# Optimization experiments

Hardware: AMD Instinct MI355X
Metric: run time of the kernel (lower is better)

The kernel has to match this reference:

```python
import jax, jax.numpy as jnp
import numpy as np

B, N, D, H, M, O = 8, 1024, 256, 512, 256, 256


def _mlp(x, W1, b1, W2, b2):
    # two-layer MLP: Linear -> ReLU -> Linear (torch Linear: x @ W.T + b)
    return jax.nn.relu(x @ W1.T + b1) @ W2.T + b2


def _lstm(x, W_ih, W_hh, b):
    # x: [B, N, D] -> h: [B, N, H]; single-layer unidirectional LSTM, torch gate order i,f,g,o
    Bt, Nt, _ = x.shape
    x_proj = x @ W_ih.T + b  # [B, N, 4H] precompute input projection

    def step(carry, xt):
        h, c = carry
        gates = xt + h @ W_hh.T
        i, f, g, o = jnp.split(gates, 4, axis=-1)
        i, f, o = jax.nn.sigmoid(i), jax.nn.sigmoid(f), jax.nn.sigmoid(o)
        c = f * c + i * jnp.tanh(g)
        h = o * jnp.tanh(c)
        return (h, c), h

    h0 = jnp.zeros((Bt, W_hh.shape[1]), x.dtype)
    (_, _), hs = jax.lax.scan(step, (h0, h0), jnp.swapaxes(x_proj, 0, 1))
    return jnp.swapaxes(hs, 0, 1)


def setup_inputs() -> dict:
    key = jax.random.key(0)
    ks = jax.random.split(key, 32)
    p = lambda k, s: jax.random.normal(k, s, jnp.float32) * 0.02
    inp = {
        "feats": jax.random.normal(ks[0], (B, N, D), jnp.float32),
        "adj": jax.random.randint(ks[1], (B, N, N), 0, 2, jnp.int32),
        "W_ih": p(ks[2], (4 * H, D)),
        "W_hh": p(ks[3], (4 * H, H)),
        "b_ih": jnp.zeros((4 * H,), jnp.float32),
        "b_hh": jnp.zeros((4 * H,), jnp.float32),
        "gx_W1": p(ks[4], (M, H)), "gx_b1": jnp.zeros((M,), jnp.float32),
        "gx_W2": p(ks[5], (M, M)), "gx_b2": jnp.zeros((M,), jnp.float32),
        "gz_W1": p(ks[6], (M, H)), "gz_b1": jnp.zeros((M,), jnp.float32),
        "gz_W2": p(ks[7], (M, M)), "gz_b2": jnp.zeros((M,), jnp.float32),
        "gv_W1": p(ks[8], (M, H)), "gv_b1": jnp.zeros((M,), jnp.float32),
        "gv_W2": p(ks[9], (M, M)), "gv_b2": jnp.zeros((M,), jnp.float32),
        "gn_W1": p(ks[10], (M, M)), "gn_b1": jnp.zeros((M,), jnp.float32),
        "gn_W2": p(ks[11], (O, M)), "gn_b2": jnp.zeros((O,), jnp.float32),
        "out_W": p(ks[12], (O, H + O)), "out_b": jnp.zeros((O,), jnp.float32),
    }
    return inp


def reference(feats, adj, W_ih, W_hh, b_ih, b_hh,
              gx_W1, gx_b1, gx_W2, gx_b2,
              gz_W1, gz_b1, gz_W2, gz_b2,
              gv_W1, gv_b1, gv_W2, gv_b2,
              gn_W1, gn_b1, gn_W2, gn_b2,
              out_W, out_b):
    h = _lstm(feats, W_ih, W_hh, b_ih + b_hh)  # [B, N, H]

    # Note: in the source, concat_1[:, :lstm_hidden_dim] == s_i and
    # concat_2[:, :lstm_hidden_dim] == s_j, so scores = <g_x(s_i), g_v(s_j)>
    ax = _mlp(h, gx_W1, gx_b1, gx_W2, gx_b2)  # [B, N, M]
    av = _mlp(h, gv_W1, gv_b1, gv_W2, gv_b2)  # [B, N, M]
    scores = jnp.einsum('bim,bjm->bij', ax, av)  # [B, N, N]

    eye = jnp.eye(N, dtype=bool)
    mask = (adj > 0) & ~eye[None]  # valid neighbors
    w = jax.nn.softmax(jnp.where(mask, scores, -1e30), axis=-1)
    w = w * mask  # zero out rows with no neighbors (softmax of all -inf -> uniform)

    sagg = jnp.einsum('bij,bjh->bih', w, h)  # weighted neighbor sum [B, N, H]
    agg = _mlp(_mlp(sagg, gz_W1, gz_b1, gz_W2, gz_b2), gn_W1, gn_b1, gn_W2, gn_b2)
    has_nb = mask.any(axis=-1, keepdims=True)  # [B, N, 1]
    agg = jnp.where(has_nb, agg, 0.0)  # isolated nodes get zero aggregate

    combined = jnp.concatenate([h, agg], axis=-1)  # [B, N, H+O]
    return combined @ out_W.T + out_b
```

## Files before the change

kernel.cpp:

```cpp
#include <hip/hip_runtime.h>

typedef unsigned short u16;
typedef unsigned long long u64;
using short8 = __attribute__((ext_vector_type(8))) short;
using f32x4  = __attribute__((ext_vector_type(4))) float;

#define GF_RELU  1
#define GF_F32   2
#define GF_XPOSE 4

__device__ __forceinline__ float b2f(u16 x) {
    unsigned u = ((unsigned)x) << 16;
    return __builtin_bit_cast(float, u);
}
__device__ __forceinline__ u16 f2b(float f) {
    unsigned u = __builtin_bit_cast(unsigned, f);
    unsigned r = u + 0x7FFFu + ((u >> 16) & 1u);
    return (u16)(r >> 16);
}
__device__ __forceinline__ f32x4 mfma_bf16(uint4 a, uint4 b, f32x4 c) {
    return __builtin_amdgcn_mfma_f32_16x16x32_bf16(
        __builtin_bit_cast(short8, a), __builtin_bit_cast(short8, b), c, 0, 0, 0);
}
__device__ __forceinline__ f32x4 zero4() { f32x4 z = {0.f, 0.f, 0.f, 0.f}; return z; }

__global__ __launch_bounds__(256) void cvt_bf16(const float* __restrict__ src,
                                                u16* __restrict__ dst, int n) {
    for (int i = blockIdx.x * 256 + threadIdx.x; i < n; i += gridDim.x * 256)
        dst[i] = f2b(src[i]);
}

__global__ void pack_params(const float* __restrict__ Whh, const float* __restrict__ Wih,
                            const float* __restrict__ bih, const float* __restrict__ bhh,
                            u16* __restrict__ WhhP, u16* __restrict__ WihP,
                            float* __restrict__ biasP) {
    int p = blockIdx.x;
    int t = threadIdx.x;
    int orig = ((p & 3) << 9) + (p >> 2);
    WhhP[((long)p << 9) + t]       = f2b(Whh[((long)orig << 9) + t]);
    WhhP[((long)p << 9) + 256 + t] = f2b(Whh[((long)orig << 9) + 256 + t]);
    WihP[((long)p << 8) + t]       = f2b(Wih[((long)orig << 8) + t]);
    if (t == 0) biasP[p] = bih[orig] + bhh[orig];
}

__global__ __launch_bounds__(256) void gemm_bt(
    const u16* __restrict__ A, const u16* __restrict__ A2, int ksplit,
    const u16* __restrict__ B, void* __restrict__ Cout,
    int M, int N, int K,
    long sAb, long sBb, long sCb,
    const float* __restrict__ bias, const float* __restrict__ rowmask, int flags) {
    __shared__ __align__(16) u16 As[64][40];
    __shared__ __align__(16) u16 Bs[128][40];
    const int bz = blockIdx.z;
    const u16* Ab = A + (long)bz * sAb;
    const u16* Bb = B + (long)bz * sBb;
    const int m0 = blockIdx.x << 6, n0 = blockIdx.y << 7;
    const int tid = threadIdx.x;
    const int lane = tid & 63, wave = tid >> 6;
    const int srow = tid >> 2, skc = (tid & 3) << 3;
    const int frm = lane & 15, fq = lane >> 4;

    auto loadA = [&](int ka) -> uint4 {
        const u16* p = (ka < ksplit)
            ? Ab + (long)(m0 + srow) * ksplit + ka
            : A2 + (long)(m0 + srow) * (K - ksplit) + (ka - ksplit);
        return *(const uint4*)p;
    };
    const u16* Brow0 = Bb + (long)(n0 + srow) * K;
    const u16* Brow1 = Bb + (long)(n0 + 64 + srow) * K;

    f32x4 acc[8];
#pragma unroll
    for (int i = 0; i < 8; i++) acc[i] = zero4();

    uint4 a  = loadA(skc);
    uint4 b0 = *(const uint4*)(Brow0 + skc);
    uint4 b1 = *(const uint4*)(Brow1 + skc);

    for (int k0 = 0; k0 < K; k0 += 32) {
        __syncthreads();
        *(uint4*)&As[srow][skc] = a;
        *(uint4*)&Bs[srow][skc] = b0;
        *(uint4*)&Bs[64 + srow][skc] = b1;
        __syncthreads();
        int kn = k0 + 32;
        if (kn < K) {
            a  = loadA(kn + skc);
            b0 = *(const uint4*)(Brow0 + kn + skc);
            b1 = *(const uint4*)(Brow1 + kn + skc);
        }
        uint4 af = *(const uint4*)&As[(wave << 4) + frm][fq << 3];
#pragma unroll
        for (int nt = 0; nt < 8; nt++) {
            uint4 bf = *(const uint4*)&Bs[(nt << 4) + frm][fq << 3];
            acc[nt] = mfma_bf16(af, bf, acc[nt]);
        }
    }
#pragma unroll
    for (int nt = 0; nt < 8; nt++) {
        int col = n0 + (nt << 4) + frm;
        float bv = bias ? bias[col] : 0.f;
#pragma unroll
        for (int r = 0; r < 4; r++) {
            int row = m0 + (wave << 4) + (fq << 2) + r;
            float v = acc[nt][r] + bv;
            if (flags & GF_RELU) v = fmaxf(v, 0.f);
            if (rowmask) v *= rowmask[row];
            long orow = (flags & GF_XPOSE) ? (long)((row & 1023) * 8 + (row >> 10))
                                           : (long)row;
            if (flags & GF_F32)
                ((float*)Cout)[(long)bz * sCb + orow * N + col] = v;
            else
                ((u16*)Cout)[(long)bz * sCb + orow * N + col] = f2b(v);
        }
    }
}

__global__ __launch_bounds__(512, 1) void lstm_rec(
    const u16* __restrict__ WhhP, const u16* __restrict__ xproj,
    u16* __restrict__ h, u64* __restrict__ hx) {
    __shared__ float g_lds[8][260];
    __shared__ unsigned hshare[8][260];
    const int wg = blockIdx.x;
    const int tid = threadIdx.x;
    const int lane = tid & 63, wv = tid >> 6;
    const int frm = lane & 15, fq = lane >> 4;
    const int mbb = frm & 7;
    const int xb = (fq & 1) << 2;
    const int ws = (wg << 3) + wv;

    uint4 bfrag[2][16];
#pragma unroll
    for (int T = 0; T < 2; T++)
#pragma unroll
        for (int kk = 0; kk < 16; kk++)
            bfrag[T][kk] = *(const uint4*)&WhhP[((long)((ws << 5) + (T << 4) + frm) << 9) +
                                                (kk << 5) + (fq << 3)];

    float creg = 0.f;
    int budget = 1 << 21;

#pragma unroll 1
    for (int t = 0; t < 1024; t++) {
        float xp[2][4];
#pragma unroll
        for (int T = 0; T < 2; T++)
#pragma unroll
            for (int r = 0; r < 4; r++)
                xp[T][r] = b2f(xproj[((long)(t * 8 + xb + r) << 11) +
                                     (ws << 5) + (T << 4) + frm]);

        f32x4 acc0 = zero4(), acc1 = zero4();
        if (t > 0) {
            const u64* buf = hx + (((t - 1) & 1) << 11);
            u64 v[4];
            const unsigned want = (unsigned)t;
            while (true) {
#pragma unroll
                for (int j = 0; j < 4; j++)
                    v[j] = __hip_atomic_load(&buf[(wv << 8) + lane + (j << 6)],
                                             __ATOMIC_RELAXED, __HIP_MEMORY_SCOPE_AGENT);
                bool ok = true;
#pragma unroll
                for (int j = 0; j < 4; j++) ok &= ((unsigned)(v[j] >> 32) == want);
                if (__all(ok) || --budget < 0) break;
            }
#pragma unroll
            for (int j = 0; j < 4; j++) {
                int a = (wv << 8) + lane + (j << 6);
                hshare[a >> 8][a & 255] = (unsigned)v[j];
            }
            __syncthreads();
            uint4 afr[16];
#pragma unroll
            for (int kk = 0; kk < 16; kk++)
                afr[kk] = *(const uint4*)&hshare[mbb][(kk << 4) + (fq << 2)];
#pragma unroll
            for (int kk = 0; kk < 16; kk++) {
                acc0 = mfma_bf16(afr[kk], bfrag[0][kk], acc0);
                acc1 = mfma_bf16(afr[kk], bfrag[1][kk], acc1);
            }
        }

        if (fq < 2) {
#pragma unroll
            for (int T = 0; T < 2; T++) {
                f32x4 accT = T ? acc1 : acc0;
#pragma unroll
                for (int r = 0; r < 4; r++)
                    g_lds[(fq << 2) + r][(wv << 5) + (T << 4) + frm] = accT[r] + xp[T][r];
            }
        }
        __syncthreads();

        {
            f32x4 g = *(const f32x4*)&g_lds[wv][lane << 2];
            float iv = 1.f / (1.f + __expf(-g[0]));
            float fv = 1.f / (1.f + __expf(-g[1]));
            float gv = 1.f - 2.f / (__expf(2.f * g[2]) + 1.f);
            float ov = 1.f / (1.f + __expf(-g[3]));
            creg = fv * creg + iv * gv;
            float hv = ov * (1.f - 2.f / (__expf(2.f * creg) + 1.f));
            float hn = __shfl_down(hv, 1);
            if (!(lane & 1)) {
                int b = wv, j = lane >> 1;
                unsigned dw = (unsigned)f2b(hv) | ((unsigned)f2b(hn) << 16);
                ((unsigned*)h)[(((long)(b * 1024 + t)) << 8) + (wg << 5) + j] = dw;
                u64 pv = ((u64)(unsigned)(t + 1) << 32) | (u64)dw;
                __hip_atomic_store(&hx[((t & 1) << 11) + (b << 8) + (wg << 5) + j], pv,
                                   __ATOMIC_RELAXED, __HIP_MEMORY_SCOPE_AGENT);
            }
        }
    }
}

__global__ __launch_bounds__(256) void transpose_h(const u16* __restrict__ h,
                                                   u16* __restrict__ hT) {
    __shared__ __align__(16) u16 tile[64][72];
    const int b = blockIdx.z;
    const int t0 = blockIdx.x << 6, u0 = blockIdx.y << 6;
    const int tid = threadIdx.x;
    const int r = tid >> 3, c8 = (tid & 7) << 3;
#pragma unroll
    for (int j = 0; j < 2; j++) {
        int row = r + (j << 5);
        *(uint4*)&tile[row][c8] =
            *(const uint4*)&h[(((long)b << 10) + t0 + row) * 512 + u0 + c8];
    }
    __syncthreads();
#pragma unroll
    for (int j = 0; j < 2; j++) {
        int urow = r + (j << 5);
        unsigned wds[4];
#pragma unroll
        for (int k = 0; k < 4; k++) {
            unsigned lo = tile[c8 + (k << 1)][urow];
            unsigned hi = tile[c8 + (k << 1) + 1][urow];
            wds[k] = lo | (hi << 16);
        }
        uint4 v; v.x = wds[0]; v.y = wds[1]; v.z = wds[2]; v.w = wds[3];
        *(uint4*)&hT[(((long)b << 9) + u0 + urow) * 1024 + t0 + c8] = v;
    }
}

__global__ __launch_bounds__(256) void softmax_row(
    const float* __restrict__ scores, const int* __restrict__ adj,
    u16* __restrict__ w, float* __restrict__ hasnb) {
    __shared__ float red[4];
    const int row = blockIdx.x;
    const int i = row & 1023;
    const int tid = threadIdx.x;
    const int lane = tid & 63, wave = tid >> 6;
    const float* s = scores + ((long)row << 10);
    const int* arow = adj + ((long)row << 10);

    float sv[4]; bool mk[4];
    float mx = -3.0e38f;
#pragma unroll
    for (int q = 0; q < 4; q++) {
        int j = tid + (q << 8);
        mk[q] = (arow[j] > 0) && (j != i);
        sv[q] = s[j];
        if (mk[q]) mx = fmaxf(mx, sv[q]);
    }
    for (int off = 32; off; off >>= 1) mx = fmaxf(mx, __shfl_xor(mx, off));
    if (lane == 0) red[wave] = mx;
    __syncthreads();
    mx = fmaxf(fmaxf(red[0], red[1]), fmaxf(red[2], red[3]));
    float e[4]; float sum = 0.f;
#pragma unroll
    for (int q = 0; q < 4; q++) {
        e[q] = mk[q] ? __expf(sv[q] - mx) : 0.f;
        sum += e[q];
    }
    __syncthreads();
    for (int off = 32; off; off >>= 1) sum += __shfl_xor(sum, off);
    if (lane == 0) red[wave] = sum;
    __syncthreads();
    sum = red[0] + red[1] + red[2] + red[3];
    float inv = sum > 0.f ? 1.f / sum : 0.f;
#pragma unroll
    for (int q = 0; q < 4; q++) {
        int j = tid + (q << 8);
        w[((long)row << 10) + j] = f2b(e[q] * inv);
    }
    if (tid == 0) hasnb[row] = sum > 0.f ? 1.f : 0.f;
}

extern "C" void kernel_launch(void* const* d_in, const int* in_sizes, int n_in,
                              void* d_out, int out_size, void* d_ws, size_t ws_size,
                              hipStream_t stream) {
    const float* feats = (const float*)d_in[0];
    const int*   adj   = (const int*)d_in[1];
    const float* W_ih  = (const float*)d_in[2];
    const float* W_hh  = (const float*)d_in[3];
    const float* b_ih  = (const float*)d_in[4];
    const float* b_hh  = (const float*)d_in[5];
    const float* gx_W1 = (const float*)d_in[6];  const float* gx_b1 = (const float*)d_in[7];
    const float* gx_W2 = (const float*)d_in[8];  const float* gx_b2 = (const float*)d_in[9];
    const float* gz_W1 = (const float*)d_in[10]; const float* gz_b1 = (const float*)d_in[11];
    const float* gz_W2 = (const float*)d_in[12]; const float* gz_b2 = (const float*)d_in[13];
    const float* gv_W1 = (const float*)d_in[14]; const float* gv_b1 = (const float*)d_in[15];
    const float* gv_W2 = (const float*)d_in[16]; const float* gv_b2 = (const float*)d_in[17];
    const float* gn_W1 = (const float*)d_in[18]; const float* gn_b1 = (const float*)d_in[19];
    const float* gn_W2 = (const float*)d_in[20]; const float* gn_b2 = (const float*)d_in[21];
    const float* out_W = (const float*)d_in[22]; const float* out_b = (const float*)d_in[23];

    char* ws = (char*)d_ws;
    size_t off = 0;
    auto alloc = [&](size_t bytes) {
        void* p = ws + off;
        off += (bytes + 255) & ~(size_t)255;
        return p;
    };
    u16* WhhP      = (u16*)alloc(2048L * 512 * 2);
    u16* WihP      = (u16*)alloc(2048L * 256 * 2);
    float* biasP   = (float*)alloc(2048L * 4);
    u64* hx        = (u64*)alloc(2L * 2048 * 8);
    u16* featsB    = (u16*)alloc(8192L * 256 * 2);
    u16* gxW1b     = (u16*)alloc(256L * 512 * 2);
    u16* gxW2b     = (u16*)alloc(256L * 256 * 2);
    u16* gvW1b     = (u16*)alloc(256L * 512 * 2);
    u16* gvW2b     = (u16*)alloc(256L * 256 * 2);
    u16* gzW1b     = (u16*)alloc(256L * 512 * 2);
    u16* gzW2b     = (u16*)alloc(256L * 256 * 2);
    u16* gnW1b     = (u16*)alloc(256L * 256 * 2);
    u16* gnW2b     = (u16*)alloc(256L * 256 * 2);
    u16* outWb     = (u16*)alloc(256L * 768 * 2);
    u16* xproj     = (u16*)alloc(8L * 1024 * 2048 * 2);
    u16* h         = (u16*)alloc(8L * 1024 * 512 * 2);
    u16* hT        = (u16*)alloc(8L * 1024 * 512 * 2);
    u16* t1        = (u16*)alloc(8192L * 256 * 2);
    u16* tB        = (u16*)alloc(8192L * 256 * 2);
    u16* ax        = (u16*)alloc(8192L * 256 * 2);
    u16* av        = (u16*)alloc(8192L * 256 * 2);
    u16* agg       = (u16*)alloc(8192L * 256 * 2);
    float* hasnb   = (float*)alloc(8192L * 4);
    float* scores  = (float*)alloc(8L * 1024 * 1024 * 4);
    u16* w         = (u16*)alloc(8L * 1024 * 1024 * 2);
    if (off > ws_size) return;

    hipMemsetAsync(hx, 0, 2L * 2048 * 8, stream);
    pack_params<<<2048, 256, 0, stream>>>(W_hh, W_ih, b_ih, b_hh, WhhP, WihP, biasP);

    auto cvt = [&](const float* src, u16* dst, int n) {
        cvt_bf16<<<(n + 1023) / 1024, 256, 0, stream>>>(src, dst, n);
    };
    cvt(feats, featsB, 8192 * 256);
    cvt(gx_W1, gxW1b, 256 * 512);  cvt(gx_W2, gxW2b, 256 * 256);
    cvt(gv_W1, gvW1b, 256 * 512);  cvt(gv_W2, gvW2b, 256 * 256);
    cvt(gz_W1, gzW1b, 256 * 512);  cvt(gz_W2, gzW2b, 256 * 256);
    cvt(gn_W1, gnW1b, 256 * 256);  cvt(gn_W2, gnW2b, 256 * 256);
    cvt(out_W, outWb, 256 * 768);

    gemm_bt<<<dim3(128, 16, 1), 256, 0, stream>>>(
        featsB, nullptr, 256, WihP, xproj, 8192, 2048, 256, 0, 0, 0,
        biasP, nullptr, GF_XPOSE);

    lstm_rec<<<8, 512, 0, stream>>>(WhhP, xproj, h, hx);

    transpose_h<<<dim3(16, 8, 8), 256, 0, stream>>>(h, hT);

    gemm_bt<<<dim3(128, 2, 1), 256, 0, stream>>>(
        h, nullptr, 512, gxW1b, t1, 8192, 256, 512, 0, 0, 0, gx_b1, nullptr, GF_RELU);
    gemm_bt<<<dim3(128, 2, 1), 256, 0, stream>>>(
        t1, nullptr, 256, gxW2b, ax, 8192, 256, 256, 0, 0, 0, gx_b2, nullptr, 0);
    gemm_bt<<<dim3(128, 2, 1), 256, 0, stream>>>(
        h, nullptr, 512, gvW1b, t1, 8192, 256, 512, 0, 0, 0, gv_b1, nullptr, GF_RELU);
    gemm_bt<<<dim3(128, 2, 1), 256, 0, stream>>>(
        t1, nullptr, 256, gvW2b, av, 8192, 256, 256, 0, 0, 0, gv_b2, nullptr, 0);

    gemm_bt<<<dim3(16, 8, 8), 256, 0, stream>>>(
        ax, nullptr, 256, av, scores, 1024, 1024, 256,
        262144, 262144, 1048576, nullptr, nullptr, GF_F32);

    softmax_row<<<8192, 256, 0, stream>>>(scores, adj, w, hasnb);

    u16* sagg = xproj;
    gemm_bt<<<dim3(16, 4, 8), 256, 0, stream>>>(
        w, nullptr, 1024, hT, sagg, 1024, 512, 1024,
        1048576, 524288, 524288, nullptr, nullptr, 0);

    gemm_bt<<<dim3(128, 2, 1), 256, 0, stream>>>(
        sagg, nullptr, 512, gzW1b, t1, 8192, 256, 512, 0, 0, 0, gz_b1, nullptr, GF_RELU);
    gemm_bt<<<dim3(128, 2, 1), 256, 0, stream>>>(
        t1, nullptr, 256, gzW2b, tB, 8192, 256, 256, 0, 0, 0, gz_b2, nullptr, 0);
    gemm_bt<<<dim3(128, 2, 1), 256, 0, stream>>>(
        tB, nullptr, 256, gnW1b, t1, 8192, 256, 256, 0, 0, 0, gn_b1, nullptr, GF_RELU);
    gemm_bt<<<dim3(128, 2, 1), 256, 0, stream>>>(
        t1, nullptr, 256, gnW2b, agg, 8192, 256, 256, 0, 0, 0, gn_b2, hasnb, 0);

    gemm_bt<<<dim3(128, 2, 1), 256, 0, stream>>>(
        h, agg, 512, outWb, (float*)d_out, 8192, 256, 768, 0, 0, 0, out_b, nullptr, GF_F32);
}
```

Measured before the change: 2.446 ms.

## Split LSTM recurrence into per-batch workgroup groups to shrink sync scope

The recurrent LSTM kernel now launches 64 workgroups instead of 8: each group of 8 workgroups handles one batch sequence, and each workgroup owns a 256-column slice of the gate matrix. The cross-workgroup h exchange buffer is partitioned per batch, so each workgroup polls only its own batch's hidden state. The per-wave LDS copy of h removes the workgroup-wide barriers. Gate accumulation is split into four independent MFMA chains, and gate values are regrouped with lane shuffles instead of an LDS round trip. The cost is that only a single batch row of each MFMA tile is useful, so matrix work is wasted, and there are more spinning workgroups.

```diff
diff --git a/kernel.cpp b/kernel.cpp
--- a/kernel.cpp
+++ b/kernel.cpp
@@ -119,46 +119,41 @@
 __global__ __launch_bounds__(512, 1) void lstm_rec(
     const u16* __restrict__ WhhP, const u16* __restrict__ xproj,
     u16* __restrict__ h, u64* __restrict__ hx) {
-    __shared__ float g_lds[8][260];
-    __shared__ unsigned hshare[8][260];
-    const int wg = blockIdx.x;
+    __shared__ __align__(16) unsigned hshare[8][256];
+    const int bid = blockIdx.x;
+    const int g = bid & 7;
+    const int s = bid >> 3;
     const int tid = threadIdx.x;
     const int lane = tid & 63, wv = tid >> 6;
     const int frm = lane & 15, fq = lane >> 4;
-    const int mbb = frm & 7;
-    const int xb = (fq & 1) << 2;
-    const int ws = (wg << 3) + wv;
+    const int colbase = (s << 8) + (wv << 5);
 
     uint4 bfrag[2][16];
 #pragma unroll
     for (int T = 0; T < 2; T++)
 #pragma unroll
         for (int kk = 0; kk < 16; kk++)
-            bfrag[T][kk] = *(const uint4*)&WhhP[((long)((ws << 5) + (T << 4) + frm) << 9) +
+            bfrag[T][kk] = *(const uint4*)&WhhP[((long)(colbase + (T << 4) + frm) << 9) +
                                                 (kk << 5) + (fq << 3)];
 
+    unsigned* hw = &hshare[wv][0];
     float creg = 0.f;
-    int budget = 1 << 21;
+    int budget = 1 << 20;
 
 #pragma unroll 1
     for (int t = 0; t < 1024; t++) {
-        float xp[2][4];
-#pragma unroll
-        for (int T = 0; T < 2; T++)
-#pragma unroll
-            for (int r = 0; r < 4; r++)
-                xp[T][r] = b2f(xproj[((long)(t * 8 + xb + r) << 11) +
-                                     (ws << 5) + (T << 4) + frm]);
-
-        f32x4 acc0 = zero4(), acc1 = zero4();
+        float xp0 = b2f(xproj[((long)(t * 8 + g) << 11) + colbase + frm]);
+        float xp1 = b2f(xproj[((long)(t * 8 + g) << 11) + colbase + 16 + frm]);
+
+        float s0, s1;
         if (t > 0) {
-            const u64* buf = hx + (((t - 1) & 1) << 11);
+            const u64* buf = hx + (g << 9) + (((t - 1) & 1) << 8);
             u64 v[4];
             const unsigned want = (unsigned)t;
             while (true) {
 #pragma unroll
                 for (int j = 0; j < 4; j++)
-                    v[j] = __hip_atomic_load(&buf[(wv << 8) + lane + (j << 6)],
+                    v[j] = __hip_atomic_load(&buf[(j << 6) + lane],
                                              __ATOMIC_RELAXED, __HIP_MEMORY_SCOPE_AGENT);
                 bool ok = true;
 #pragma unroll
@@ -166,50 +161,52 @@
                 if (__all(ok) || --budget < 0) break;
             }
 #pragma unroll
-            for (int j = 0; j < 4; j++) {
-                int a = (wv << 8) + lane + (j << 6);
-                hshare[a >> 8][a & 255] = (unsigned)v[j];
+            for (int j = 0; j < 4; j++) hw[(j << 6) + lane] = (unsigned)v[j];
+
+            f32x4 a0p[4], a1p[4];
+#pragma unroll
+            for (int r = 0; r < 4; r++) { a0p[r] = zero4(); a1p[r] = zero4(); }
+#pragma unroll
+            for (int r4 = 0; r4 < 4; r4++) {
+                uint4 af[4];
+#pragma unroll
+                for (int q = 0; q < 4; q++)
+                    af[q] = *(const uint4*)&hw[(((r4 << 2) | q) << 4) + (fq << 2)];
+#pragma unroll
+                for (int q = 0; q < 4; q++) {
+                    a0p[r4] = mfma_bf16(af[q], bfrag[0][(r4 << 2) | q], a0p[r4]);
+                    a1p[r4] = mfma_bf16(af[q], bfrag[1][(r4 << 2) | q], a1p[r4]);
+                }
             }
-            __syncthreads();
-            uint4 afr[16];
-#pragma unroll
-            for (int kk = 0; kk < 16; kk++)
-                afr[kk] = *(const uint4*)&hshare[mbb][(kk << 4) + (fq << 2)];
-#pragma unroll
-            for (int kk = 0; kk < 16; kk++) {
-                acc0 = mfma_bf16(afr[kk], bfrag[0][kk], acc0);
-                acc1 = mfma_bf16(afr[kk], bfrag[1][kk], acc1);
-            }
-        }
-
-        if (fq < 2) {
-#pragma unroll
-            for (int T = 0; T < 2; T++) {
-                f32x4 accT = T ? acc1 : acc0;
-#pragma unroll
-                for (int r = 0; r < 4; r++)
-                    g_lds[(fq << 2) + r][(wv << 5) + (T << 4) + frm] = accT[r] + xp[T][r];
-            }
-        }
-        __syncthreads();
-
-        {
-            f32x4 g = *(const f32x4*)&g_lds[wv][lane << 2];
-            float iv = 1.f / (1.f + __expf(-g[0]));
-            float fv = 1.f / (1.f + __expf(-g[1]));
-            float gv = 1.f - 2.f / (__expf(2.f * g[2]) + 1.f);
-            float ov = 1.f / (1.f + __expf(-g[3]));
-            creg = fv * creg + iv * gv;
-            float hv = ov * (1.f - 2.f / (__expf(2.f * creg) + 1.f));
-            float hn = __shfl_down(hv, 1);
-            if (!(lane & 1)) {
-                int b = wv, j = lane >> 1;
-                unsigned dw = (unsigned)f2b(hv) | ((unsigned)f2b(hn) << 16);
-                ((unsigned*)h)[(((long)(b * 1024 + t)) << 8) + (wg << 5) + j] = dw;
-                u64 pv = ((u64)(unsigned)(t + 1) << 32) | (u64)dw;
-                __hip_atomic_store(&hx[((t & 1) << 11) + (b << 8) + (wg << 5) + j], pv,
-                                   __ATOMIC_RELAXED, __HIP_MEMORY_SCOPE_AGENT);
-            }
+            s0 = (a0p[0][0] + a0p[1][0]) + (a0p[2][0] + a0p[3][0]) + xp0;
+            s1 = (a1p[0][0] + a1p[1][0]) + (a1p[2][0] + a1p[3][0]) + xp1;
+        } else {
+            s0 = xp0;
+            s1 = xp1;
+        }
+
+        float ss[4];
+#pragma unroll
+        for (int k = 0; k < 4; k++) {
+            int src = ((lane << 2) + k) & 15;
+            float t0 = __shfl(s0, src);
+            float t1 = __shfl(s1, src);
+            ss[k] = (lane < 4) ? t0 : t1;
+        }
+        float iv = 1.f / (1.f + __expf(-ss[0]));
+        float fv = 1.f / (1.f + __expf(-ss[1]));
+        float gv = 1.f - 2.f / (__expf(2.f * ss[2]) + 1.f);
+        float ov = 1.f / (1.f + __expf(-ss[3]));
+        creg = fv * creg + iv * gv;
+        float hv = ov * (1.f - 2.f / (__expf(2.f * creg) + 1.f));
+        float hn = __shfl_down(hv, 1);
+        if (lane < 8 && !(lane & 1)) {
+            unsigned dw = (unsigned)f2b(hv) | ((unsigned)f2b(hn) << 16);
+            int d = (s << 5) + (wv << 2) + (lane >> 1);
+            ((unsigned*)h)[(((long)(g * 1024 + t)) << 8) + d] = dw;
+            u64 pv = ((u64)(unsigned)(t + 1) << 32) | (u64)dw;
+            __hip_atomic_store(&hx[(g << 9) + ((t & 1) << 8) + d], pv,
+                               __ATOMIC_RELAXED, __HIP_MEMORY_SCOPE_AGENT);
         }
     }
 }
@@ -316,7 +313,7 @@
     u16* WhhP      = (u16*)alloc(2048L * 512 * 2);
     u16* WihP      = (u16*)alloc(2048L * 256 * 2);
     float* biasP   = (float*)alloc(2048L * 4);
-    u64* hx        = (u64*)alloc(2L * 2048 * 8);
+    u64* hx        = (u64*)alloc(8L * 512 * 8);
     u16* featsB    = (u16*)alloc(8192L * 256 * 2);
     u16* gxW1b     = (u16*)alloc(256L * 512 * 2);
     u16* gxW2b     = (u16*)alloc(256L * 256 * 2);
@@ -340,7 +337,7 @@
     u16* w         = (u16*)alloc(8L * 1024 * 1024 * 2);
     if (off > ws_size) return;
 
-    hipMemsetAsync(hx, 0, 2L * 2048 * 8, stream);
+    hipMemsetAsync(hx, 0, 8L * 512 * 8, stream);
     pack_params<<<2048, 256, 0, stream>>>(W_hh, W_ih, b_ih, b_hh, WhhP, WihP, biasP);
 
     auto cvt = [&](const float* src, u16* dst, int n) {
@@ -357,7 +354,7 @@
         featsB, nullptr, 256, WihP, xproj, 8192, 2048, 256, 0, 0, 0,
         biasP, nullptr, GF_XPOSE);
 
-    lstm_rec<<<8, 512, 0, stream>>>(WhhP, xproj, h, hx);
+    lstm_rec<<<64, 512, 0, stream>>>(WhhP, xproj, h, hx);
 
     transpose_h<<<dim3(16, 8, 8), 256, 0, stream>>>(h, hT);
 
```

Result: slower. 2.607 ms (+6.6%).
